# Performance work log

Hardware: AMD Instinct MI355X
Metric: run time of the kernel (lower is better)

## Reference

```python
import jax, jax.numpy as jnp
import numpy as np

B, T, S, D = 8, 2048, 2048, 1024

def setup_inputs() -> dict:
    key = jax.random.key(0)
    k1, k2 = jax.random.split(key)
    trg_outs = jax.random.normal(k1, (B, T, D), dtype=jnp.float32)
    src_outs = jax.random.normal(k2, (B, S, D), dtype=jnp.float32)
    return {"trg_outs": trg_outs, "src_outs": src_outs}

def reference(trg_outs, src_outs):
    # Luong 'dot' attention: unscaled dot-product scores.
    # scores: (B, T, S)
    attn_scores = jnp.einsum('btd,bsd->bts', trg_outs, src_outs)
    attn_weights = jax.nn.softmax(attn_scores, axis=2)
    # context: (B, T, D)
    context_vec = jnp.einsum('bts,bsd->btd', attn_weights, src_outs)
    return (context_vec, attn_weights)
```

## Files before the change

kernel.cpp:

```cpp
#include <hip/hip_runtime.h>


#define BB 8
#define TT 2048
#define SS 2048
#define DD 1024

typedef float  f32x4   __attribute__((ext_vector_type(4)));
typedef float  f32x16  __attribute__((ext_vector_type(16)));
typedef short  bf16x8  __attribute__((ext_vector_type(8)));
typedef _Float16 f16x8 __attribute__((ext_vector_type(8)));
typedef _Float16 f16x4 __attribute__((ext_vector_type(4)));

static __device__ __forceinline__ unsigned short bf16_rne(float x) {
  unsigned int u = __float_as_uint(x);
  u += 0x7FFFu + ((u >> 16) & 1u);
  return (unsigned short)(u >> 16);
}

static __device__ __forceinline__ void gl2lds16(const void* g, void* l) {
  __builtin_amdgcn_global_load_lds(
      (const __attribute__((address_space(1))) unsigned int*)g,
      (__attribute__((address_space(3))) unsigned int*)l, 16, 0, 0);
}

__global__ __launch_bounds__(256)
void conv_trg_f16(const float* __restrict__ x, _Float16* __restrict__ h16) {
  const size_t i = ((size_t)blockIdx.x * 256 + threadIdx.x) * 8;
  float4 v0 = *(const float4*)(x + i);
  float4 v1 = *(const float4*)(x + i + 4);
  f16x8 h;
  h[0] = (_Float16)v0.x; h[1] = (_Float16)v0.y;
  h[2] = (_Float16)v0.z; h[3] = (_Float16)v0.w;
  h[4] = (_Float16)v1.x; h[5] = (_Float16)v1.y;
  h[6] = (_Float16)v1.z; h[7] = (_Float16)v1.w;
  *(f16x8*)(h16 + i) = h;
}

__global__ __launch_bounds__(256)
void conv_src_f16_hilo_t(const float* __restrict__ src,
                         _Float16* __restrict__ hi,
                         _Float16* __restrict__ lo,
                         _Float16* __restrict__ srcT) {
  const int b  = blockIdx.z;
  const int d0 = blockIdx.x * 64;
  const int s0 = blockIdx.y * 64;
  const float* S = src + (size_t)b * SS * DD;
  __shared__ _Float16 t16[64][65];
  const int t = threadIdx.x;

#pragma unroll
  for (int p = 0; p < 4; ++p) {
    const int r = p * 16 + (t >> 4);
    const int c = (t & 15) * 4;
    float4 v = *(const float4*)(S + (size_t)(s0 + r) * DD + d0 + c);
    float f[4] = {v.x, v.y, v.z, v.w};
    f16x4 h, l;
#pragma unroll
    for (int e = 0; e < 4; ++e) {
      _Float16 hv = (_Float16)f[e];
      h[e] = hv;
      l[e] = (_Float16)(f[e] - (float)hv);
      t16[r][c + e] = hv;
    }
    const size_t go = ((size_t)b * SS + s0 + r) * DD + d0 + c;
    *(f16x4*)(hi + go) = h;
    *(f16x4*)(lo + go) = l;
  }
  __syncthreads();
#pragma unroll
  for (int p = 0; p < 4; ++p) {
    const int d  = p * 16 + (t >> 4);
    const int sq = (t & 15) * 4;
    f16x4 o;
#pragma unroll
    for (int k = 0; k < 4; ++k) o[k] = t16[sq + k][d];
    *(f16x4*)(srcT + ((size_t)b * DD + d0 + d) * SS + s0 + sq) = o;
  }
}

__global__ __launch_bounds__(256, 1)
void attn_gemm1_2p(const _Float16* __restrict__ a16,
                   const _Float16* __restrict__ bh16,
                   const _Float16* __restrict__ bl16,
                   float* __restrict__ scores) {
  const int b   = blockIdx.z;
  const int tm0 = blockIdx.y * 128;
  const int tn0 = blockIdx.x * 128;
  float* C = scores + (size_t)b * TT * SS;

  __shared__ __align__(16) _Float16 smA[4096];
  __shared__ __align__(16) _Float16 smBh[4096], smBl[4096];

  const int t      = threadIdx.x;
  const int lane   = t & 63;
  const int wv     = t >> 6;
  const int m_off  = (wv & 1) * 64;
  const int n_off  = (wv >> 1) * 64;
  const int lrow32 = lane & 31;
  const int khalf  = lane >> 5;

  const int s0 = t, s1 = t + 256;
  const int r0 = s0 >> 2, g0 = (s0 & 3) ^ ((r0 >> 1) & 3);
  const int r1 = s1 >> 2, g1 = (s1 & 3) ^ ((r1 >> 1) & 3);

  const _Float16* pA0 = a16 + ((size_t)b * TT + tm0 + r0) * DD + g0 * 8;
  const _Float16* pA1 = a16 + ((size_t)b * TT + tm0 + r1) * DD + g1 * 8;
  const _Float16* pBh0 = bh16 + ((size_t)b * SS + tn0 + r0) * DD + g0 * 8;
  const _Float16* pBh1 = bh16 + ((size_t)b * SS + tn0 + r1) * DD + g1 * 8;
  const _Float16* pBl0 = bl16 + ((size_t)b * SS + tn0 + r0) * DD + g0 * 8;
  const _Float16* pBl1 = bl16 + ((size_t)b * SS + tn0 + r1) * DD + g1 * 8;

  f32x16 acc[2][2];
#pragma unroll
  for (int i = 0; i < 2; ++i)
#pragma unroll
    for (int j = 0; j < 2; ++j) acc[i][j] = (f32x16)0.0f;

  for (int kt = 0; kt < DD; kt += 32) {
    __syncthreads();
    gl2lds16(pA0, smA + s0 * 8);  gl2lds16(pA1, smA + s1 * 8);
    gl2lds16(pBh0, smBh + s0 * 8); gl2lds16(pBh1, smBh + s1 * 8);
    gl2lds16(pBl0, smBl + s0 * 8); gl2lds16(pBl1, smBl + s1 * 8);
    pA0 += 32; pA1 += 32; pBh0 += 32; pBh1 += 32; pBl0 += 32; pBl1 += 32;
    __syncthreads();

#pragma unroll
    for (int kk = 0; kk < 2; ++kk) {
      const int cb = kk * 2 + khalf;
      f16x8 a[2], bh[2], bl[2];
#pragma unroll
      for (int mi = 0; mi < 2; ++mi) {
        const int r   = m_off + mi * 32 + lrow32;
        const int off = (r * 4 + (cb ^ ((r >> 1) & 3))) * 8;
        a[mi] = *(const f16x8*)(smA + off);
      }
#pragma unroll
      for (int ni = 0; ni < 2; ++ni) {
        const int r   = n_off + ni * 32 + lrow32;
        const int off = (r * 4 + (cb ^ ((r >> 1) & 3))) * 8;
        bh[ni] = *(const f16x8*)(smBh + off);
        bl[ni] = *(const f16x8*)(smBl + off);
      }
#pragma unroll
      for (int mi = 0; mi < 2; ++mi)
#pragma unroll
        for (int ni = 0; ni < 2; ++ni) {
          acc[mi][ni] = __builtin_amdgcn_mfma_f32_32x32x16_f16(a[mi], bh[ni], acc[mi][ni], 0, 0, 0);
          acc[mi][ni] = __builtin_amdgcn_mfma_f32_32x32x16_f16(a[mi], bl[ni], acc[mi][ni], 0, 0, 0);
        }
    }
  }

  const int rsub = 4 * khalf;
#pragma unroll
  for (int mi = 0; mi < 2; ++mi)
#pragma unroll
    for (int ni = 0; ni < 2; ++ni) {
      const int rb  = tm0 + m_off + mi * 32 + rsub;
      const int col = tn0 + n_off + ni * 32 + lrow32;
#pragma unroll
      for (int p = 0; p < 16; ++p)
        C[(size_t)(rb + (p & 3) + 8 * (p >> 2)) * SS + col] = acc[mi][ni][p];
    }
}

__global__ __launch_bounds__(64)
void attn_softmax_w16(float* __restrict__ w, _Float16* __restrict__ w16) {
  const size_t row = blockIdx.x;
  float4* p4 = (float4*)(w + row * SS);
  _Float16* o = w16 + row * SS;
  const int lane = threadIdx.x;

  float4 v[8];
#pragma unroll
  for (int j = 0; j < 8; ++j) v[j] = p4[lane + 64 * j];

  float m = -1e30f;
#pragma unroll
  for (int j = 0; j < 8; ++j)
    m = fmaxf(m, fmaxf(fmaxf(v[j].x, v[j].y), fmaxf(v[j].z, v[j].w)));
#pragma unroll
  for (int off = 32; off >= 1; off >>= 1) m = fmaxf(m, __shfl_xor(m, off, 64));

  float s = 0.0f;
#pragma unroll
  for (int j = 0; j < 8; ++j) {
    v[j].x = __expf(v[j].x - m); v[j].y = __expf(v[j].y - m);
    v[j].z = __expf(v[j].z - m); v[j].w = __expf(v[j].w - m);
    s += v[j].x + v[j].y + v[j].z + v[j].w;
  }
#pragma unroll
  for (int off = 32; off >= 1; off >>= 1) s += __shfl_xor(s, off, 64);

  const float inv = __fdividef(1.0f, s);
#pragma unroll
  for (int j = 0; j < 8; ++j) {
    v[j].x *= inv; v[j].y *= inv; v[j].z *= inv; v[j].w *= inv;
    p4[lane + 64 * j] = v[j];
    f16x4 h;
    h[0] = (_Float16)v[j].x; h[1] = (_Float16)v[j].y;
    h[2] = (_Float16)v[j].z; h[3] = (_Float16)v[j].w;
    *(f16x4*)(o + 4 * (lane + 64 * j)) = h;
  }
}

__global__ __launch_bounds__(256, 1)
void attn_gemm2_fast32(const _Float16* __restrict__ w16,
                       const _Float16* __restrict__ srcT,
                       float* __restrict__ out) {
  const int b   = blockIdx.z;
  const int tm0 = blockIdx.y * 128;
  const int tn0 = blockIdx.x * 128;
  float* C = out + (size_t)b * TT * DD;

  __shared__ __align__(16) _Float16 smA[4096], smB[4096];

  const int t      = threadIdx.x;
  const int lane   = t & 63;
  const int wv     = t >> 6;
  const int m_off  = (wv & 1) * 64;
  const int n_off  = (wv >> 1) * 64;
  const int lrow32 = lane & 31;
  const int khalf  = lane >> 5;

  const int s0 = t, s1 = t + 256;
  const int r0 = s0 >> 2, g0 = (s0 & 3) ^ ((r0 >> 1) & 3);
  const int r1 = s1 >> 2, g1 = (s1 & 3) ^ ((r1 >> 1) & 3);

  const _Float16* pA0 = w16 + ((size_t)b * TT + tm0 + r0) * SS + g0 * 8;
  const _Float16* pA1 = w16 + ((size_t)b * TT + tm0 + r1) * SS + g1 * 8;
  const _Float16* pB0 = srcT + ((size_t)b * DD + tn0 + r0) * SS + g0 * 8;
  const _Float16* pB1 = srcT + ((size_t)b * DD + tn0 + r1) * SS + g1 * 8;

  f32x16 acc[2][2];
#pragma unroll
  for (int i = 0; i < 2; ++i)
#pragma unroll
    for (int j = 0; j < 2; ++j) acc[i][j] = (f32x16)0.0f;

  for (int kt = 0; kt < SS; kt += 32) {
    __syncthreads();
    gl2lds16(pA0, smA + s0 * 8); gl2lds16(pA1, smA + s1 * 8);
    gl2lds16(pB0, smB + s0 * 8); gl2lds16(pB1, smB + s1 * 8);
    pA0 += 32; pA1 += 32; pB0 += 32; pB1 += 32;
    __syncthreads();

#pragma unroll
    for (int kk = 0; kk < 2; ++kk) {
      const int cb = kk * 2 + khalf;
      f16x8 af[2], bf[2];
#pragma unroll
      for (int mi = 0; mi < 2; ++mi) {
        const int r   = m_off + mi * 32 + lrow32;
        const int off = (r * 4 + (cb ^ ((r >> 1) & 3))) * 8;
        af[mi] = *(const f16x8*)(smA + off);
      }
#pragma unroll
      for (int ni = 0; ni < 2; ++ni) {
        const int r   = n_off + ni * 32 + lrow32;
        const int off = (r * 4 + (cb ^ ((r >> 1) & 3))) * 8;
        bf[ni] = *(const f16x8*)(smB + off);
      }
#pragma unroll
      for (int mi = 0; mi < 2; ++mi)
#pragma unroll
        for (int ni = 0; ni < 2; ++ni)
          acc[mi][ni] = __builtin_amdgcn_mfma_f32_32x32x16_f16(af[mi], bf[ni], acc[mi][ni], 0, 0, 0);
    }
  }

  const int rsub = 4 * khalf;
#pragma unroll
  for (int mi = 0; mi < 2; ++mi)
#pragma unroll
    for (int ni = 0; ni < 2; ++ni) {
      const int rb  = tm0 + m_off + mi * 32 + rsub;
      const int col = tn0 + n_off + ni * 32 + lrow32;
#pragma unroll
      for (int p = 0; p < 16; ++p)
        C[(size_t)(rb + (p & 3) + 8 * (p >> 2)) * DD + col] = acc[mi][ni][p];
    }
}

__global__ __launch_bounds__(256, 1)
void attn_gemm1_scores_bf16x3(const float* __restrict__ trg,
                              const float* __restrict__ src,
                              float* __restrict__ scores) {
  const int b   = blockIdx.z;
  const int tm0 = blockIdx.y * 128;
  const int tn0 = blockIdx.x * 128;
  const float* A  = trg + (size_t)b * TT * DD;
  const float* Bm = src + (size_t)b * SS * DD;
  float* C = scores + (size_t)b * TT * SS;

  __shared__ __align__(16) unsigned short smAh[128 * 32];
  __shared__ __align__(16) unsigned short smAl[128 * 32];
  __shared__ __align__(16) unsigned short smBh[128 * 32];
  __shared__ __align__(16) unsigned short smBl[128 * 32];

  const int t     = threadIdx.x;
  const int lane  = t & 63;
  const int wv    = t >> 6;
  const int m_off = (wv & 1) * 64;
  const int n_off = (wv >> 1) * 64;
  const int q     = lane >> 4;
  const int lrow  = lane & 15;

  f32x4 acc[4][4];
#pragma unroll
  for (int i = 0; i < 4; ++i)
#pragma unroll
    for (int j = 0; j < 4; ++j) acc[i][j] = (f32x4)0.0f;

  for (int kt = 0; kt < DD; kt += 32) {
    __syncthreads();
#pragma unroll
    for (int h = 0; h < 2; ++h) {
      const int c  = t + h * 256;
      const int r  = c >> 2;
      const int j  = c & 3;
      const int gk = j ^ ((r >> 1) & 3);
      {
        const float* ga = A + (size_t)(tm0 + r) * DD + kt + gk * 8;
        float4 v0 = *(const float4*)ga;
        float4 v1 = *(const float4*)(ga + 4);
        float f[8] = {v0.x, v0.y, v0.z, v0.w, v1.x, v1.y, v1.z, v1.w};
        bf16x8 hi, lo;
#pragma unroll
        for (int e = 0; e < 8; ++e) {
          unsigned short hb = bf16_rne(f[e]);
          hi[e] = (short)hb;
          float hf = __uint_as_float(((unsigned int)hb) << 16);
          lo[e] = (short)bf16_rne(f[e] - hf);
        }
        *(bf16x8*)(smAh + c * 8) = hi;
        *(bf16x8*)(smAl + c * 8) = lo;
      }
      {
        const float* gb = Bm + (size_t)(tn0 + r) * DD + kt + gk * 8;
        float4 v0 = *(const float4*)gb;
        float4 v1 = *(const float4*)(gb + 4);
        float f[8] = {v0.x, v0.y, v0.z, v0.w, v1.x, v1.y, v1.z, v1.w};
        bf16x8 hi, lo;
#pragma unroll
        for (int e = 0; e < 8; ++e) {
          unsigned short hb = bf16_rne(f[e]);
          hi[e] = (short)hb;
          float hf = __uint_as_float(((unsigned int)hb) << 16);
          lo[e] = (short)bf16_rne(f[e] - hf);
        }
        *(bf16x8*)(smBh + c * 8) = hi;
        *(bf16x8*)(smBl + c * 8) = lo;
      }
    }
    __syncthreads();

    bf16x8 ah[4], al[4], bh[4], bl[4];
#pragma unroll
    for (int mi = 0; mi < 4; ++mi) {
      const int r   = m_off + mi * 16 + lrow;
      const int off = (r * 4 + (q ^ ((r >> 1) & 3))) * 8;
      ah[mi] = *(const bf16x8*)(smAh + off);
      al[mi] = *(const bf16x8*)(smAl + off);
    }
#pragma unroll
    for (int ni = 0; ni < 4; ++ni) {
      const int r   = n_off + ni * 16 + lrow;
      const int off = (r * 4 + (q ^ ((r >> 1) & 3))) * 8;
      bh[ni] = *(const bf16x8*)(smBh + off);
      bl[ni] = *(const bf16x8*)(smBl + off);
    }
#pragma unroll
    for (int mi = 0; mi < 4; ++mi)
#pragma unroll
      for (int ni = 0; ni < 4; ++ni) {
        acc[mi][ni] = __builtin_amdgcn_mfma_f32_16x16x32_bf16(al[mi], bh[ni], acc[mi][ni], 0, 0, 0);
        acc[mi][ni] = __builtin_amdgcn_mfma_f32_16x16x32_bf16(ah[mi], bl[ni], acc[mi][ni], 0, 0, 0);
        acc[mi][ni] = __builtin_amdgcn_mfma_f32_16x16x32_bf16(ah[mi], bh[ni], acc[mi][ni], 0, 0, 0);
      }
  }

#pragma unroll
  for (int mi = 0; mi < 4; ++mi)
#pragma unroll
    for (int ni = 0; ni < 4; ++ni) {
      const int row0 = tm0 + m_off + mi * 16 + q * 4;
      const int col  = tn0 + n_off + ni * 16 + lrow;
#pragma unroll
      for (int p = 0; p < 4; ++p)
        C[(size_t)(row0 + p) * SS + col] = acc[mi][ni][p];
    }
}

__global__ __launch_bounds__(256)
void attn_softmax_rows(float* __restrict__ w) {
  float* p = w + (size_t)blockIdx.x * SS;
  const int t = threadIdx.x;
  float4* p4 = (float4*)p;
  float4 v0 = p4[t];
  float4 v1 = p4[t + 256];

  float m = fmaxf(fmaxf(fmaxf(v0.x, v0.y), fmaxf(v0.z, v0.w)),
                  fmaxf(fmaxf(v1.x, v1.y), fmaxf(v1.z, v1.w)));
#pragma unroll
  for (int off = 32; off >= 1; off >>= 1) m = fmaxf(m, __shfl_xor(m, off, 64));
  __shared__ float redm[4];
  __shared__ float reds[4];
  const int wv = t >> 6, lane = t & 63;
  if (lane == 0) redm[wv] = m;
  __syncthreads();
  m = fmaxf(fmaxf(redm[0], redm[1]), fmaxf(redm[2], redm[3]));

  v0.x = __expf(v0.x - m); v0.y = __expf(v0.y - m);
  v0.z = __expf(v0.z - m); v0.w = __expf(v0.w - m);
  v1.x = __expf(v1.x - m); v1.y = __expf(v1.y - m);
  v1.z = __expf(v1.z - m); v1.w = __expf(v1.w - m);

  float s = v0.x + v0.y + v0.z + v0.w + v1.x + v1.y + v1.z + v1.w;
#pragma unroll
  for (int off = 32; off >= 1; off >>= 1) s += __shfl_xor(s, off, 64);
  if (lane == 0) reds[wv] = s;
  __syncthreads();
  s = reds[0] + reds[1] + reds[2] + reds[3];

  const float inv = __fdividef(1.0f, s);
  v0.x *= inv; v0.y *= inv; v0.z *= inv; v0.w *= inv;
  v1.x *= inv; v1.y *= inv; v1.z *= inv; v1.w *= inv;
  p4[t] = v0;
  p4[t + 256] = v1;
}

__global__ __launch_bounds__(256, 1)
void attn_gemm2_ctx_f16(const float* __restrict__ w,
                        const float* __restrict__ src,
                        float* __restrict__ out) {
  const int b   = blockIdx.z;
  const int tm0 = blockIdx.y * 128;
  const int tn0 = blockIdx.x * 128;
  const float* A  = w + (size_t)b * TT * SS;
  const float* Bs = src + (size_t)b * SS * DD;
  float* C = out + (size_t)b * TT * DD;

  __shared__ __align__(16) _Float16 smA[128 * 32];
  __shared__ __align__(16) _Float16 smB[128 * 32];

  const int t     = threadIdx.x;
  const int lane  = t & 63;
  const int wv    = t >> 6;
  const int m_off = (wv & 1) * 64;
  const int n_off = (wv >> 1) * 64;
  const int q     = lane >> 4;
  const int lrow  = lane & 15;

  const int bn    = t & 127;
  const int bh2   = t >> 7;
  const int bs2   = (bn >> 1) & 3;
  const int slot0 = (2 * bh2) ^ bs2;
  const int slot1 = (2 * bh2 + 1) ^ bs2;

  f32x4 acc[4][4];
#pragma unroll
  for (int i = 0; i < 4; ++i)
#pragma unroll
    for (int j = 0; j < 4; ++j) acc[i][j] = (f32x4)0.0f;

  for (int kt = 0; kt < SS; kt += 32) {
    __syncthreads();
#pragma unroll
    for (int h = 0; h < 2; ++h) {
      const int c  = t + h * 256;
      const int r  = c >> 2;
      const int j  = c & 3;
      const int gk = j ^ ((r >> 1) & 3);
      const float* ga = A + (size_t)(tm0 + r) * SS + kt + gk * 8;
      float4 v0 = *(const float4*)ga;
      float4 v1 = *(const float4*)(ga + 4);
      f16x8 hv;
      hv[0] = (_Float16)v0.x; hv[1] = (_Float16)v0.y;
      hv[2] = (_Float16)v0.z; hv[3] = (_Float16)v0.w;
      hv[4] = (_Float16)v1.x; hv[5] = (_Float16)v1.y;
      hv[6] = (_Float16)v1.z; hv[7] = (_Float16)v1.w;
      *(f16x8*)(smA + c * 8) = hv;
    }
    {
      const float* gb = Bs + (size_t)(kt + bh2 * 16) * DD + (tn0 + bn);
      f16x8 c0, c1;
#pragma unroll
      for (int kk = 0; kk < 8; ++kk) c0[kk] = (_Float16)gb[(size_t)kk * DD];
#pragma unroll
      for (int kk = 0; kk < 8; ++kk) c1[kk] = (_Float16)gb[(size_t)(kk + 8) * DD];
      *(f16x8*)(smB + bn * 32 + slot0 * 8) = c0;
      *(f16x8*)(smB + bn * 32 + slot1 * 8) = c1;
    }
    __syncthreads();

    f16x8 af[4], bfr[4];
#pragma unroll
    for (int mi = 0; mi < 4; ++mi) {
      const int r   = m_off + mi * 16 + lrow;
      const int off = (r * 4 + (q ^ ((r >> 1) & 3))) * 8;
      af[mi] = *(const f16x8*)(smA + off);
    }
#pragma unroll
    for (int ni = 0; ni < 4; ++ni) {
      const int n   = n_off + ni * 16 + lrow;
      const int off = n * 32 + (q ^ ((n >> 1) & 3)) * 8;
      bfr[ni] = *(const f16x8*)(smB + off);
    }
#pragma unroll
    for (int mi = 0; mi < 4; ++mi)
#pragma unroll
      for (int ni = 0; ni < 4; ++ni)
        acc[mi][ni] = __builtin_amdgcn_mfma_f32_16x16x32_f16(af[mi], bfr[ni], acc[mi][ni], 0, 0, 0);
  }

#pragma unroll
  for (int mi = 0; mi < 4; ++mi)
#pragma unroll
    for (int ni = 0; ni < 4; ++ni) {
      const int row0 = tm0 + m_off + mi * 16 + q * 4;
      const int col  = tn0 + n_off + ni * 16 + lrow;
#pragma unroll
      for (int p = 0; p < 4; ++p)
        C[(size_t)(row0 + p) * DD + col] = acc[mi][ni][p];
    }
}

extern "C" void kernel_launch(void* const* d_in, const int* in_sizes, int n_in,
                              void* d_out, int out_size, void* d_ws, size_t ws_size,
                              hipStream_t stream) {
  const float* trg = (const float*)d_in[0];
  const float* src = (const float*)d_in[1];
  float* ctx = (float*)d_out;
  float* wts = (float*)d_out + (size_t)BB * TT * DD;

  const size_t NT = (size_t)BB * TT * DD;
  const size_t NW = (size_t)BB * TT * SS;
  const size_t need = (4 * NT + NW) * 2;

  if (ws_size >= need) {
    _Float16* tH16 = (_Float16*)d_ws;
    _Float16* sH16 = tH16 + NT;
    _Float16* sL16 = sH16 + NT;
    _Float16* srcT = sL16 + NT;
    _Float16* w16  = srcT + NT;

    conv_trg_f16<<<dim3(NT / (8 * 256)), 256, 0, stream>>>(trg, tH16);
    conv_src_f16_hilo_t<<<dim3(DD / 64, SS / 64, BB), 256, 0, stream>>>(src, sH16, sL16, srcT);
    attn_gemm1_2p<<<dim3(SS / 128, TT / 128, BB), 256, 0, stream>>>(tH16, sH16, sL16, wts);
    attn_softmax_w16<<<dim3(BB * TT), 64, 0, stream>>>(wts, w16);
    attn_gemm2_fast32<<<dim3(DD / 128, TT / 128, BB), 256, 0, stream>>>(w16, srcT, ctx);
  } else {
    attn_gemm1_scores_bf16x3<<<dim3(SS / 128, TT / 128, BB), 256, 0, stream>>>(trg, src, wts);
    attn_softmax_rows<<<dim3(BB * TT), 256, 0, stream>>>(wts);
    attn_gemm2_ctx_f16<<<dim3(DD / 128, TT / 128, BB), 256, 0, stream>>>(wts, src, ctx);
  }
}
```

Baseline: 594.6 us.

## Triple-buffer LDS pipelining with 256x256 tiles in both attention GEMMs

```diff
diff --git a/kernel.cpp b/kernel.cpp
--- a/kernel.cpp
+++ b/kernel.cpp
@@ -79,86 +79,116 @@
   }
 }
 
-__global__ __launch_bounds__(256, 1)
-void attn_gemm1_2p(const _Float16* __restrict__ a16,
-                   const _Float16* __restrict__ bh16,
-                   const _Float16* __restrict__ bl16,
-                   float* __restrict__ scores) {
+__global__ __launch_bounds__(512, 2)
+void attn_gemm1_pipe(const _Float16* __restrict__ a16,
+                     const _Float16* __restrict__ bh16,
+                     const _Float16* __restrict__ bl16,
+                     float* __restrict__ scores) {
   const int b   = blockIdx.z;
-  const int tm0 = blockIdx.y * 128;
-  const int tn0 = blockIdx.x * 128;
+  const int tm0 = blockIdx.y * 256;
+  const int tn0 = blockIdx.x * 256;
   float* C = scores + (size_t)b * TT * SS;
 
-  __shared__ __align__(16) _Float16 smA[4096];
-  __shared__ __align__(16) _Float16 smBh[4096], smBl[4096];
+  __shared__ __align__(16) _Float16 sm[3][3][8192];
 
   const int t      = threadIdx.x;
   const int lane   = t & 63;
   const int wv     = t >> 6;
-  const int m_off  = (wv & 1) * 64;
-  const int n_off  = (wv >> 1) * 64;
+  const int wm     = (wv >> 2) * 128;
+  const int wn     = (wv & 3) * 64;
   const int lrow32 = lane & 31;
   const int khalf  = lane >> 5;
 
-  const int s0 = t, s1 = t + 256;
+  const int s0 = t, s1 = t + 512;
   const int r0 = s0 >> 2, g0 = (s0 & 3) ^ ((r0 >> 1) & 3);
   const int r1 = s1 >> 2, g1 = (s1 & 3) ^ ((r1 >> 1) & 3);
 
-  const _Float16* pA0 = a16 + ((size_t)b * TT + tm0 + r0) * DD + g0 * 8;
-  const _Float16* pA1 = a16 + ((size_t)b * TT + tm0 + r1) * DD + g1 * 8;
+  const _Float16* pA0  = a16  + ((size_t)b * TT + tm0 + r0) * DD + g0 * 8;
+  const _Float16* pA1  = a16  + ((size_t)b * TT + tm0 + r1) * DD + g1 * 8;
   const _Float16* pBh0 = bh16 + ((size_t)b * SS + tn0 + r0) * DD + g0 * 8;
   const _Float16* pBh1 = bh16 + ((size_t)b * SS + tn0 + r1) * DD + g1 * 8;
   const _Float16* pBl0 = bl16 + ((size_t)b * SS + tn0 + r0) * DD + g0 * 8;
   const _Float16* pBl1 = bl16 + ((size_t)b * SS + tn0 + r1) * DD + g1 * 8;
 
-  f32x16 acc[2][2];
-#pragma unroll
-  for (int i = 0; i < 2; ++i)
+#define STAGE1(dst)                                    \
+  do {                                                 \
+    gl2lds16(pA0,  (dst) + s0 * 8);                    \
+    gl2lds16(pA1,  (dst) + s1 * 8);                    \
+    gl2lds16(pBh0, (dst) + 8192 + s0 * 8);             \
+    gl2lds16(pBh1, (dst) + 8192 + s1 * 8);             \
+    gl2lds16(pBl0, (dst) + 16384 + s0 * 8);            \
+    gl2lds16(pBl1, (dst) + 16384 + s1 * 8);            \
+    pA0 += 32; pA1 += 32; pBh0 += 32; pBh1 += 32;      \
+    pBl0 += 32; pBl1 += 32;                            \
+  } while (0)
+
+  f32x16 acc[4][2];
+#pragma unroll
+  for (int i = 0; i < 4; ++i)
 #pragma unroll
     for (int j = 0; j < 2; ++j) acc[i][j] = (f32x16)0.0f;
 
-  for (int kt = 0; kt < DD; kt += 32) {
-    __syncthreads();
-    gl2lds16(pA0, smA + s0 * 8);  gl2lds16(pA1, smA + s1 * 8);
-    gl2lds16(pBh0, smBh + s0 * 8); gl2lds16(pBh1, smBh + s1 * 8);
-    gl2lds16(pBl0, smBl + s0 * 8); gl2lds16(pBl1, smBl + s1 * 8);
-    pA0 += 32; pA1 += 32; pBh0 += 32; pBh1 += 32; pBl0 += 32; pBl1 += 32;
-    __syncthreads();
-
+  _Float16* bufc = &sm[0][0][0];
+  _Float16* bufo = &sm[1][0][0];
+  _Float16* bufn = &sm[2][0][0];
+
+  STAGE1(bufc);
+  STAGE1(bufo);
+  asm volatile("s_waitcnt vmcnt(6)" ::: "memory");
+  __builtin_amdgcn_s_barrier();
+  __builtin_amdgcn_sched_barrier(0);
+
+  const int NT = DD / 32;
+#pragma unroll 1
+  for (int tt = 0; tt < NT; ++tt) {
+    if (tt + 2 < NT) STAGE1(bufn);
+
+    const _Float16* As = bufc;
+    const _Float16* Bh = bufc + 8192;
+    const _Float16* Bl = bufc + 16384;
 #pragma unroll
     for (int kk = 0; kk < 2; ++kk) {
       const int cb = kk * 2 + khalf;
-      f16x8 a[2], bh[2], bl[2];
-#pragma unroll
-      for (int mi = 0; mi < 2; ++mi) {
-        const int r   = m_off + mi * 32 + lrow32;
+      f16x8 a[4], bh[2], bl[2];
+#pragma unroll
+      for (int mi = 0; mi < 4; ++mi) {
+        const int r = wm + mi * 32 + lrow32;
+        a[mi] = *(const f16x8*)(As + (r * 4 + (cb ^ ((r >> 1) & 3))) * 8);
+      }
+#pragma unroll
+      for (int ni = 0; ni < 2; ++ni) {
+        const int r   = wn + ni * 32 + lrow32;
         const int off = (r * 4 + (cb ^ ((r >> 1) & 3))) * 8;
-        a[mi] = *(const f16x8*)(smA + off);
+        bh[ni] = *(const f16x8*)(Bh + off);
+        bl[ni] = *(const f16x8*)(Bl + off);
       }
-#pragma unroll
-      for (int ni = 0; ni < 2; ++ni) {
-        const int r   = n_off + ni * 32 + lrow32;
-        const int off = (r * 4 + (cb ^ ((r >> 1) & 3))) * 8;
-        bh[ni] = *(const f16x8*)(smBh + off);
-        bl[ni] = *(const f16x8*)(smBl + off);
-      }
-#pragma unroll
-      for (int mi = 0; mi < 2; ++mi)
+      __builtin_amdgcn_s_setprio(1);
+#pragma unroll
+      for (int mi = 0; mi < 4; ++mi)
 #pragma unroll
         for (int ni = 0; ni < 2; ++ni) {
           acc[mi][ni] = __builtin_amdgcn_mfma_f32_32x32x16_f16(a[mi], bh[ni], acc[mi][ni], 0, 0, 0);
           acc[mi][ni] = __builtin_amdgcn_mfma_f32_32x32x16_f16(a[mi], bl[ni], acc[mi][ni], 0, 0, 0);
         }
-    }
-  }
+      __builtin_amdgcn_s_setprio(0);
+    }
+
+    if (tt + 2 < NT) asm volatile("s_waitcnt vmcnt(6)" ::: "memory");
+    else             asm volatile("s_waitcnt vmcnt(0)" ::: "memory");
+    __builtin_amdgcn_s_barrier();
+    __builtin_amdgcn_sched_barrier(0);
+
+    _Float16* tmp = bufc; bufc = bufo; bufo = bufn; bufn = tmp;
+  }
+#undef STAGE1
 
   const int rsub = 4 * khalf;
 #pragma unroll
-  for (int mi = 0; mi < 2; ++mi)
+  for (int mi = 0; mi < 4; ++mi)
 #pragma unroll
     for (int ni = 0; ni < 2; ++ni) {
-      const int rb  = tm0 + m_off + mi * 32 + rsub;
-      const int col = tn0 + n_off + ni * 32 + lrow32;
+      const int rb  = tm0 + wm + mi * 32 + rsub;
+      const int col = tn0 + wn + ni * 32 + lrow32;
 #pragma unroll
       for (int p = 0; p < 16; ++p)
         C[(size_t)(rb + (p & 3) + 8 * (p >> 2)) * SS + col] = acc[mi][ni][p];
@@ -205,78 +235,105 @@
   }
 }
 
-__global__ __launch_bounds__(256, 1)
-void attn_gemm2_fast32(const _Float16* __restrict__ w16,
-                       const _Float16* __restrict__ srcT,
-                       float* __restrict__ out) {
+__global__ __launch_bounds__(512, 2)
+void attn_gemm2_pipe(const _Float16* __restrict__ w16,
+                     const _Float16* __restrict__ srcT,
+                     float* __restrict__ out) {
   const int b   = blockIdx.z;
-  const int tm0 = blockIdx.y * 128;
-  const int tn0 = blockIdx.x * 128;
+  const int tm0 = blockIdx.y * 256;
+  const int tn0 = blockIdx.x * 256;
   float* C = out + (size_t)b * TT * DD;
 
-  __shared__ __align__(16) _Float16 smA[4096], smB[4096];
+  __shared__ __align__(16) _Float16 sm[3][2][8192];
 
   const int t      = threadIdx.x;
   const int lane   = t & 63;
   const int wv     = t >> 6;
-  const int m_off  = (wv & 1) * 64;
-  const int n_off  = (wv >> 1) * 64;
+  const int wm     = (wv >> 2) * 128;
+  const int wn     = (wv & 3) * 64;
   const int lrow32 = lane & 31;
   const int khalf  = lane >> 5;
 
-  const int s0 = t, s1 = t + 256;
+  const int s0 = t, s1 = t + 512;
   const int r0 = s0 >> 2, g0 = (s0 & 3) ^ ((r0 >> 1) & 3);
   const int r1 = s1 >> 2, g1 = (s1 & 3) ^ ((r1 >> 1) & 3);
 
-  const _Float16* pA0 = w16 + ((size_t)b * TT + tm0 + r0) * SS + g0 * 8;
-  const _Float16* pA1 = w16 + ((size_t)b * TT + tm0 + r1) * SS + g1 * 8;
+  const _Float16* pA0 = w16  + ((size_t)b * TT + tm0 + r0) * SS + g0 * 8;
+  const _Float16* pA1 = w16  + ((size_t)b * TT + tm0 + r1) * SS + g1 * 8;
   const _Float16* pB0 = srcT + ((size_t)b * DD + tn0 + r0) * SS + g0 * 8;
   const _Float16* pB1 = srcT + ((size_t)b * DD + tn0 + r1) * SS + g1 * 8;
 
-  f32x16 acc[2][2];
-#pragma unroll
-  for (int i = 0; i < 2; ++i)
+#define STAGE2(dst)                                    \
+  do {                                                 \
+    gl2lds16(pA0, (dst) + s0 * 8);                     \
+    gl2lds16(pA1, (dst) + s1 * 8);                     \
+    gl2lds16(pB0, (dst) + 8192 + s0 * 8);              \
+    gl2lds16(pB1, (dst) + 8192 + s1 * 8);              \
+    pA0 += 32; pA1 += 32; pB0 += 32; pB1 += 32;        \
+  } while (0)
+
+  f32x16 acc[4][2];
+#pragma unroll
+  for (int i = 0; i < 4; ++i)
 #pragma unroll
     for (int j = 0; j < 2; ++j) acc[i][j] = (f32x16)0.0f;
 
-  for (int kt = 0; kt < SS; kt += 32) {
-    __syncthreads();
-    gl2lds16(pA0, smA + s0 * 8); gl2lds16(pA1, smA + s1 * 8);
-    gl2lds16(pB0, smB + s0 * 8); gl2lds16(pB1, smB + s1 * 8);
-    pA0 += 32; pA1 += 32; pB0 += 32; pB1 += 32;
-    __syncthreads();
-
+  _Float16* bufc = &sm[0][0][0];
+  _Float16* bufo = &sm[1][0][0];
+  _Float16* bufn = &sm[2][0][0];
+
+  STAGE2(bufc);
+  STAGE2(bufo);
+  asm volatile("s_waitcnt vmcnt(4)" ::: "memory");
+  __builtin_amdgcn_s_barrier();
+  __builtin_amdgcn_sched_barrier(0);
+
+  const int NT = SS / 32;
+#pragma unroll 1
+  for (int tt = 0; tt < NT; ++tt) {
+    if (tt + 2 < NT) STAGE2(bufn);
+
+    const _Float16* As = bufc;
+    const _Float16* Bs = bufc + 8192;
 #pragma unroll
     for (int kk = 0; kk < 2; ++kk) {
       const int cb = kk * 2 + khalf;
-      f16x8 af[2], bf[2];
-#pragma unroll
-      for (int mi = 0; mi < 2; ++mi) {
-        const int r   = m_off + mi * 32 + lrow32;
-        const int off = (r * 4 + (cb ^ ((r >> 1) & 3))) * 8;
-        af[mi] = *(const f16x8*)(smA + off);
+      f16x8 a[4], bf[2];
+#pragma unroll
+      for (int mi = 0; mi < 4; ++mi) {
+        const int r = wm + mi * 32 + lrow32;
+        a[mi] = *(const f16x8*)(As + (r * 4 + (cb ^ ((r >> 1) & 3))) * 8);
       }
 #pragma unroll
       for (int ni = 0; ni < 2; ++ni) {
-        const int r   = n_off + ni * 32 + lrow32;
-        const int off = (r * 4 + (cb ^ ((r >> 1) & 3))) * 8;
-        bf[ni] = *(const f16x8*)(smB + off);
+        const int r = wn + ni * 32 + lrow32;
+        bf[ni] = *(const f16x8*)(Bs + (r * 4 + (cb ^ ((r >> 1) & 3))) * 8);
       }
-#pragma unroll
-      for (int mi = 0; mi < 2; ++mi)
+      __builtin_amdgcn_s_setprio(1);
+#pragma unroll
+      for (int mi = 0; mi < 4; ++mi)
 #pragma unroll
         for (int ni = 0; ni < 2; ++ni)
-          acc[mi][ni] = __builtin_amdgcn_mfma_f32_32x32x16_f16(af[mi], bf[ni], acc[mi][ni], 0, 0, 0);
-    }
-  }
+          acc[mi][ni] = __builtin_amdgcn_mfma_f32_32x32x16_f16(a[mi], bf[ni], acc[mi][ni], 0, 0, 0);
+      __builtin_amdgcn_s_setprio(0);
+    }
+
+    if (tt + 2 < NT) asm volatile("s_waitcnt vmcnt(4)" ::: "memory");
+    else             asm volatile("s_waitcnt vmcnt(0)" ::: "memory");
+    __builtin_amdgcn_s_barrier();
+    __builtin_amdgcn_sched_barrier(0);
+
+    _Float16* tmp = bufc; bufc = bufo; bufo = bufn; bufn = tmp;
+  }
+#undef STAGE2
 
   const int rsub = 4 * khalf;
 #pragma unroll
-  for (int mi = 0; mi < 2; ++mi)
+  for (int mi = 0; mi < 4; ++mi)
 #pragma unroll
     for (int ni = 0; ni < 2; ++ni) {
-      const int rb  = tm0 + m_off + mi * 32 + rsub;
-      const int col = tn0 + n_off + ni * 32 + lrow32;
+      const int rb  = tm0 + wm + mi * 32 + rsub;
+      const int col = tn0 + wn + ni * 32 + lrow32;
 #pragma unroll
       for (int p = 0; p < 16; ++p)
         C[(size_t)(rb + (p & 3) + 8 * (p >> 2)) * DD + col] = acc[mi][ni][p];
@@ -548,9 +605,9 @@
 
     conv_trg_f16<<<dim3(NT / (8 * 256)), 256, 0, stream>>>(trg, tH16);
     conv_src_f16_hilo_t<<<dim3(DD / 64, SS / 64, BB), 256, 0, stream>>>(src, sH16, sL16, srcT);
-    attn_gemm1_2p<<<dim3(SS / 128, TT / 128, BB), 256, 0, stream>>>(tH16, sH16, sL16, wts);
+    attn_gemm1_pipe<<<dim3(SS / 256, TT / 256, BB), 512, 0, stream>>>(tH16, sH16, sL16, wts);
     attn_softmax_w16<<<dim3(BB * TT), 64, 0, stream>>>(wts, w16);
-    attn_gemm2_fast32<<<dim3(DD / 128, TT / 128, BB), 256, 0, stream>>>(w16, srcT, ctx);
+    attn_gemm2_pipe<<<dim3(DD / 256, TT / 256, BB), 512, 0, stream>>>(w16, srcT, ctx);
   } else {
     attn_gemm1_scores_bf16x3<<<dim3(SS / 128, TT / 128, BB), 256, 0, stream>>>(trg, src, wts);
     attn_softmax_rows<<<dim3(BB * TT), 256, 0, stream>>>(wts);
```

After: 558.6 us. 6.1% less time.
